# Performance work log

Hardware: AMD Instinct MI355X
Metric: run time of the kernel (lower is better)

Reference implementation:

```python
import jax, jax.numpy as jnp
import numpy as np

DIM = 2048
HEADS = 16
DIM_HEAD = 128
DIM_INNER = HEADS * DIM_HEAD
BATCH = 2
SEQ = 2048
EPS = 1e-12  # F.normalize default eps


def l2norm(t, axis=-1):
    # matches F.normalize(t, dim=axis, p=2): t / max(||t||, eps)
    n = jnp.sqrt(jnp.sum(t * t, axis=axis, keepdims=True))
    return t / jnp.maximum(n, EPS)


def setup_inputs() -> dict:
    key = jax.random.key(0)
    ks = jax.random.split(key, 5)
    x = jax.random.normal(ks[0], (BATCH, SEQ, DIM), dtype=jnp.float32)
    # NormLinear weights (torch Linear layout: [out, in]); parametrization
    # l2-normalizes rows (dim=-1) for q/k/v and columns (dim=0) for to_out.
    Wq = jax.random.normal(ks[1], (DIM_INNER, DIM), dtype=jnp.float32) / np.sqrt(DIM)
    Wk = jax.random.normal(ks[2], (DIM_INNER, DIM), dtype=jnp.float32) / np.sqrt(DIM)
    Wv = jax.random.normal(ks[3], (DIM_INNER, DIM), dtype=jnp.float32) / np.sqrt(DIM)
    Wout = jax.random.normal(ks[4], (DIM, DIM_INNER), dtype=jnp.float32) / np.sqrt(DIM_INNER)
    # Scale(dim_inner, init=1.0, scale=dim**-1): param = ones * dim**-1,
    # forward_scale = init/scale = dim, so qk_scale() starts at 1.0
    qk_scale = jnp.ones((DIM_INNER,), dtype=jnp.float32) / DIM
    return {"x": x, "Wq": Wq, "Wk": Wk, "Wv": Wv, "Wout": Wout, "qk_scale": qk_scale}


def reference(x, Wq, Wk, Wv, Wout, qk_scale):
    b, n, _ = x.shape
    # NormLinear: x @ l2norm(W, rows).T  (scale = groups**-1 = 1)
    q = jnp.einsum('bnd,ed->bne', x, l2norm(Wq, axis=-1))
    k = jnp.einsum('bnd,ed->bne', x, l2norm(Wk, axis=-1))
    v = jnp.einsum('bnd,ed->bne', x, l2norm(Wv, axis=-1))
    # split heads: b n (h d) -> b h n d
    split = lambda t: t.reshape(b, n, HEADS, DIM_HEAD).transpose(0, 2, 1, 3)
    q, k, v = split(q), split(k), split(v)
    # per-head l2norm of q and k over head dim
    q = l2norm(q, axis=-1)
    k = l2norm(k, axis=-1)
    # learned qk scale: (h d) -> h 1 d, effective = param * forward_scale(=DIM)
    q = q * (qk_scale * DIM).reshape(HEADS, 1, DIM_HEAD)
    # causal SDPA with scale = sqrt(dim_head) (unit-norm q,k in nGPT)
    attn_scale = DIM_HEAD ** 0.5
    scores = jnp.einsum('bhid,bhjd->bhij', q, k) * attn_scale
    causal = jnp.tril(jnp.ones((n, n), dtype=bool))
    scores = jnp.where(causal, scores, jnp.finfo(scores.dtype).min)
    attn = jax.nn.softmax(scores, axis=-1)
    out = jnp.einsum('bhij,bhjd->bhid', attn, v)
    # merge heads: b h n d -> b n (h d)
    out = out.transpose(0, 2, 1, 3).reshape(b, n, DIM_INNER)
    # to_out: NormLinear with norm over dim=0 of weight [DIM, DIM_INNER]
    out = jnp.einsum('bne,de->bnd', out, l2norm(Wout, axis=0))
    return out
```

## Files before the change

kernel.cpp:

```cpp
#include <hip/hip_runtime.h>


typedef __bf16 bf16x8 __attribute__((ext_vector_type(8)));
typedef float f32x4 __attribute__((ext_vector_type(4)));

__device__ __forceinline__ unsigned short f2bf(float f) {
  unsigned int u = __float_as_uint(f);
  u = u + 0x7FFFu + ((u >> 16) & 1u);
  return (unsigned short)(u >> 16);
}

__device__ __forceinline__ void async16(const void* g, void* l) {
  __builtin_amdgcn_global_load_lds(
      (const __attribute__((address_space(1))) unsigned int*)g,
      (__attribute__((address_space(3))) unsigned int*)l, 16, 0, 0);
}

#define QFOLD (2048.0f * 11.313708498984761f * 1.4426950408889634f)

__global__ __launch_bounds__(256) void prep_all(
    const float* __restrict__ x, const float* __restrict__ Wq,
    const float* __restrict__ Wk, const float* __restrict__ Wv,
    const float* __restrict__ qks, ushort* __restrict__ xbf,
    ushort* __restrict__ wqn, ushort* __restrict__ wkn,
    ushort* __restrict__ wvn, float* __restrict__ colss,
    float* __restrict__ mh) {
  const int bid = blockIdx.x;
  const int t = threadIdx.x;
  if (bid < 6144) {
    const int z = bid >> 11, row = bid & 2047;
    const float* W = (z == 0) ? Wq : (z == 1) ? Wk : Wv;
    ushort* O = (z == 0) ? wqn : (z == 1) ? wkn : wvn;
    const float4* Wr = (const float4*)(W + (size_t)row * 2048);
    float4 v0 = Wr[t];
    float4 v1 = Wr[t + 256];
    float ss = v0.x * v0.x + v0.y * v0.y + v0.z * v0.z + v0.w * v0.w +
               v1.x * v1.x + v1.y * v1.y + v1.z * v1.z + v1.w * v1.w;
    ss += __shfl_xor(ss, 1);  ss += __shfl_xor(ss, 2);
    ss += __shfl_xor(ss, 4);  ss += __shfl_xor(ss, 8);
    ss += __shfl_xor(ss, 16); ss += __shfl_xor(ss, 32);
    __shared__ float red[4];
    if ((t & 63) == 0) red[t >> 6] = ss;
    __syncthreads();
    float tot = red[0] + red[1] + red[2] + red[3];
    float sc = 1.0f / fmaxf(sqrtf(tot), 1e-12f);
    ushort4 o0, o1;
    o0.x = f2bf(v0.x * sc); o0.y = f2bf(v0.y * sc);
    o0.z = f2bf(v0.z * sc); o0.w = f2bf(v0.w * sc);
    o1.x = f2bf(v1.x * sc); o1.y = f2bf(v1.y * sc);
    o1.z = f2bf(v1.z * sc); o1.w = f2bf(v1.w * sc);
    *(ushort4*)(O + (size_t)row * 2048 + t * 4) = o0;
    *(ushort4*)(O + (size_t)row * 2048 + 1024 + t * 4) = o1;
  } else if (bid < 14336) {
    const int idx = ((bid - 6144) * 256 + t) * 4;
    float4 v = *(const float4*)(x + idx);
    ushort4 o;
    o.x = f2bf(v.x); o.y = f2bf(v.y); o.z = f2bf(v.z); o.w = f2bf(v.w);
    *(ushort4*)(xbf + idx) = o;
  } else if (bid < 14352) {
    const int h = bid - 14336;
    if (t < 64) {
      const int l = t;
      float m = fmaxf(fabsf(qks[h * 128 + l]), fabsf(qks[h * 128 + 64 + l]));
      m = fmaxf(m, __shfl_xor(m, 1));  m = fmaxf(m, __shfl_xor(m, 2));
      m = fmaxf(m, __shfl_xor(m, 4));  m = fmaxf(m, __shfl_xor(m, 8));
      m = fmaxf(m, __shfl_xor(m, 16)); m = fmaxf(m, __shfl_xor(m, 32));
      if (l == 0) mh[h] = m * QFOLD;
    }
  } else {
    float4 z4 = (float4){0.f, 0.f, 0.f, 0.f};
    ((float4*)colss)[t] = z4;
    ((float4*)colss)[t + 256] = z4;
  }
}

__global__ __launch_bounds__(256) void wout_colss(const float* __restrict__ W,
                                                  float* __restrict__ colss) {
  const int e = blockIdx.x * 256 + threadIdx.x;
  const int d0 = blockIdx.y * 128;
  float ss = 0.f;
  #pragma unroll 8
  for (int i = 0; i < 128; ++i) {
    float v = W[(size_t)(d0 + i) * 2048 + e];
    ss += v * v;
  }
  atomicAdd(colss + e, ss);
}

__global__ __launch_bounds__(256) void wout_norm(const float* __restrict__ W,
                                                 const float* __restrict__ colss,
                                                 ushort* __restrict__ O) {
  const int idx = (blockIdx.x * 256 + threadIdx.x) * 4;
  float4 v = *(const float4*)(W + idx);
  float4 c = *(const float4*)(colss + (idx & 2047));
  ushort4 o;
  o.x = f2bf(v.x / fmaxf(sqrtf(c.x), 1e-12f));
  o.y = f2bf(v.y / fmaxf(sqrtf(c.y), 1e-12f));
  o.z = f2bf(v.z / fmaxf(sqrtf(c.z), 1e-12f));
  o.w = f2bf(v.w / fmaxf(sqrtf(c.w), 1e-12f));
  *(ushort4*)(O + idx) = o;
}

__device__ __forceinline__ void gemm_mainloop(
    const ushort* __restrict__ A, const ushort* __restrict__ Bw,
    int m0, int n0, ushort* As, ushort* Bs, f32x4 acc[4][4],
    int t, int l, int wm, int wn) {
  const int l15 = l & 15, l4 = l >> 4;
  const ushort* abase = A + (size_t)m0 * 2048;
  const ushort* bbase = Bw + (size_t)n0 * 2048;
  for (int kt = 0; kt < 32; ++kt) {
    const int k0 = kt * 64;
    __syncthreads();
    #pragma unroll
    for (int p = 0; p < 9; ++p) {
      int c = p * 256 + t;
      const ushort* src = abase;
      char* dst = (char*)As;
      int cc = c;
      if (c >= 1152) { cc = c - 1152; src = bbase; dst = (char*)Bs; }
      int r = cc / 9, dc = cc - r * 9;
      int dcc = (dc == 8) ? 0 : dc;
      async16(src + (size_t)r * 2048 + k0 + dcc * 8, dst + cc * 16);
    }
    __syncthreads();
    #pragma unroll
    for (int ks = 0; ks < 2; ++ks) {
      bf16x8 af[4], bg[4];
      #pragma unroll
      for (int f = 0; f < 4; ++f)
        af[f] = *(const bf16x8*)&As[(wm * 64 + f * 16 + l15) * 72 + ks * 32 + l4 * 8];
      #pragma unroll
      for (int f = 0; f < 4; ++f)
        bg[f] = *(const bf16x8*)&Bs[(wn * 64 + f * 16 + l15) * 72 + ks * 32 + l4 * 8];
      #pragma unroll
      for (int fm = 0; fm < 4; ++fm)
        #pragma unroll
        for (int fn = 0; fn < 4; ++fn)
          acc[fm][fn] = __builtin_amdgcn_mfma_f32_16x16x32_bf16(
              af[fm], bg[fn], acc[fm][fn], 0, 0, 0);
    }
  }
}

__global__ __launch_bounds__(256, 4) void gemm_qkv(
    const ushort* __restrict__ X, const ushort* __restrict__ Wq,
    const ushort* __restrict__ Wk, const ushort* __restrict__ Wv,
    const float* __restrict__ qks, ushort* __restrict__ qn,
    ushort* __restrict__ kn, ushort* __restrict__ vt) {
  const int z = blockIdx.z;
  const ushort* Bw = (z == 0) ? Wq : (z == 1) ? Wk : Wv;
  const int n0 = blockIdx.x * 128;
  const int m0 = blockIdx.y * 128;
  __shared__ __align__(16) ushort As[128 * 72];
  __shared__ __align__(16) ushort Bs[128 * 72];
  __shared__ float partials[2][128];
  const int t = threadIdx.x, w = t >> 6, l = t & 63;
  const int wm = w & 1, wn = w >> 1;
  const int l15 = l & 15, l4 = l >> 4;

  f32x4 acc[4][4];
  #pragma unroll
  for (int i = 0; i < 4; ++i)
    #pragma unroll
    for (int j = 0; j < 4; ++j) acc[i][j] = (f32x4){0.f, 0.f, 0.f, 0.f};

  gemm_mainloop(X, Bw, m0, n0, As, Bs, acc, t, l, wm, wn);

  const int h = n0 >> 7;
  if (z == 2) {
    #pragma unroll
    for (int fm = 0; fm < 4; ++fm) {
      int mrow = m0 + wm * 64 + fm * 16 + l4 * 4;
      int bb = mrow >> 11;
      int nn = mrow & 2047;
      #pragma unroll
      for (int fn = 0; fn < 4; ++fn) {
        int d = wn * 64 + fn * 16 + l15;
        ushort4 p;
        p.x = f2bf(acc[fm][fn][0]); p.y = f2bf(acc[fm][fn][1]);
        p.z = f2bf(acc[fm][fn][2]); p.w = f2bf(acc[fm][fn][3]);
        *(ushort4*)(vt + (size_t)((bb * 16 + h) * 128 + d) * 2048 + nn) = p;
      }
    }
  } else {
    float rs[4][4];
    #pragma unroll
    for (int fm = 0; fm < 4; ++fm)
      #pragma unroll
      for (int r = 0; r < 4; ++r) {
        float s = 0.f;
        #pragma unroll
        for (int fn = 0; fn < 4; ++fn) {
          float v = acc[fm][fn][r];
          s += v * v;
        }
        s += __shfl_xor(s, 1); s += __shfl_xor(s, 2);
        s += __shfl_xor(s, 4); s += __shfl_xor(s, 8);
        rs[fm][r] = s;
      }
    if (l15 == 0) {
      #pragma unroll
      for (int fm = 0; fm < 4; ++fm)
        #pragma unroll
        for (int r = 0; r < 4; ++r)
          partials[wn][wm * 64 + fm * 16 + l4 * 4 + r] = rs[fm][r];
    }
    __syncthreads();
    float cs[4];
    #pragma unroll
    for (int fn = 0; fn < 4; ++fn)
      cs[fn] = (z == 0) ? qks[n0 + wn * 64 + fn * 16 + l15] * QFOLD : 1.0f;
    ushort* O = (z == 0) ? qn : kn;
    #pragma unroll
    for (int fm = 0; fm < 4; ++fm)
      #pragma unroll
      for (int r = 0; r < 4; ++r) {
        int i = wm * 64 + fm * 16 + l4 * 4 + r;
        float tot = partials[0][i] + partials[1][i];
        float sc = 1.0f / fmaxf(sqrtf(tot), 1e-12f);
        #pragma unroll
        for (int fn = 0; fn < 4; ++fn)
          O[(size_t)(m0 + i) * 2048 + n0 + wn * 64 + fn * 16 + l15] =
              f2bf(acc[fm][fn][r] * sc * cs[fn]);
      }
  }
}


#define LDSBUF 49152
#define ABYTES 32768

__device__ __forceinline__ void mainloop_256x128(
    const ushort* __restrict__ A, const ushort* __restrict__ Bw,
    int m0, int n0, char* lds, f32x4 acc[4][4], int t) {
  const int l = t & 63, w = t >> 6;
  const int wm = w & 3, wn = w >> 2;
  const int l15 = l & 15, l4 = l >> 4;

  const int lc = (t & 7) ^ ((t >> 3) & 7);
  const ushort* srcA = A + (size_t)m0 * 2048 + (t >> 3) * 2048 + lc * 8;
  const ushort* srcB = Bw + (size_t)n0 * 2048 + (t >> 3) * 2048 + lc * 8;
  char* dstA = lds + t * 16;
  char* dstB = lds + ABYTES + t * 16;

  const int rdA = (wm * 64 + l15) * 128;
  const int rdB = ABYTES + (wn * 64 + l15) * 128;
  const int cb0 = ((l4 ^ (l15 & 7)) * 16);
  const int cb1 = (((4 + l4) ^ (l15 & 7)) * 16);

  auto stageA = [&](int s, int k0, int o) {
    async16(srcA + (size_t)o * 131072 + k0, dstA + s * LDSBUF + o * 8192);
  };
  auto stageB = [&](int s, int k0, int o) {
    async16(srcB + (size_t)o * 131072 + k0, dstB + s * LDSBUF + o * 8192);
  };

  #pragma unroll
  for (int i = 0; i < 4; ++i)
    #pragma unroll
    for (int j = 0; j < 4; ++j) acc[i][j] = (f32x4){0.f, 0.f, 0.f, 0.f};

  stageA(0, 0, 0); stageA(0, 0, 1); stageA(0, 0, 2); stageA(0, 0, 3);
  stageB(0, 0, 0); stageB(0, 0, 1);
  stageA(1, 64, 0); stageA(1, 64, 1); stageA(1, 64, 2); stageA(1, 64, 3);
  stageB(1, 64, 0); stageB(1, 64, 1);
  asm volatile("s_waitcnt vmcnt(6)" ::: "memory");
  __builtin_amdgcn_s_barrier();

  auto tile = [&](int s, int s2, int k2, bool pf) {
    const char* Ab = lds + s * LDSBUF;
    bf16x8 af[4][2], bg[4][2];
    #pragma unroll
    for (int fm = 0; fm < 4; ++fm) {
      af[fm][0] = *(const bf16x8*)(Ab + rdA + fm * 2048 + cb0);
      af[fm][1] = *(const bf16x8*)(Ab + rdA + fm * 2048 + cb1);
    }
    #pragma unroll
    for (int fn = 0; fn < 2; ++fn) {
      bg[fn][0] = *(const bf16x8*)(Ab + rdB + fn * 2048 + cb0);
      bg[fn][1] = *(const bf16x8*)(Ab + rdB + fn * 2048 + cb1);
    }
    if (pf) { stageA(s2, k2, 0); stageA(s2, k2, 1); stageA(s2, k2, 2); }
    __builtin_amdgcn_s_setprio(1);
    #pragma unroll
    for (int ks = 0; ks < 2; ++ks)
      #pragma unroll
      for (int fm = 0; fm < 4; ++fm)
        #pragma unroll
        for (int fn = 0; fn < 2; ++fn)
          acc[fm][fn] = __builtin_amdgcn_mfma_f32_16x16x32_bf16(
              af[fm][ks], bg[fn][ks], acc[fm][fn], 0, 0, 0);
    __builtin_amdgcn_s_setprio(0);
    #pragma unroll
    for (int fn = 2; fn < 4; ++fn) {
      bg[fn][0] = *(const bf16x8*)(Ab + rdB + fn * 2048 + cb0);
      bg[fn][1] = *(const bf16x8*)(Ab + rdB + fn * 2048 + cb1);
    }
    if (pf) { stageA(s2, k2, 3); stageB(s2, k2, 0); stageB(s2, k2, 1); }
    __builtin_amdgcn_s_setprio(1);
    #pragma unroll
    for (int ks = 0; ks < 2; ++ks)
      #pragma unroll
      for (int fm = 0; fm < 4; ++fm)
        #pragma unroll
        for (int fn = 2; fn < 4; ++fn)
          acc[fm][fn] = __builtin_amdgcn_mfma_f32_16x16x32_bf16(
              af[fm][ks], bg[fn][ks], acc[fm][fn], 0, 0, 0);
    __builtin_amdgcn_s_setprio(0);
  };

  #pragma unroll 1
  for (int kt = 0; kt < 30; kt += 3) {
    tile(0, 2, (kt + 2) * 64, true);
    asm volatile("s_waitcnt vmcnt(6)" ::: "memory");
    __builtin_amdgcn_s_barrier();
    tile(1, 0, (kt + 3) * 64, true);
    asm volatile("s_waitcnt vmcnt(6)" ::: "memory");
    __builtin_amdgcn_s_barrier();
    tile(2, 1, (kt + 4) * 64, true);
    asm volatile("s_waitcnt vmcnt(6)" ::: "memory");
    __builtin_amdgcn_s_barrier();
  }
  tile(0, 0, 0, false);
  asm volatile("s_waitcnt vmcnt(0)" ::: "memory");
  __builtin_amdgcn_s_barrier();
  tile(1, 0, 0, false);
}

__global__ __launch_bounds__(256, 3) void attn_kernel(
    const ushort* __restrict__ qn, const ushort* __restrict__ kn,
    const ushort* __restrict__ vt, const float* __restrict__ mhead,
    ushort* __restrict__ ao) {
  const int hb = blockIdx.x;
  const int b = hb >> 4, h = hb & 15;
  const int qt = 31 - blockIdx.y;
  const int i0 = qt * 64;
  const int t = threadIdx.x, w = t >> 6, l = t & 63;
  const int l15 = l & 15, l4 = l >> 4;

  __shared__ __align__(16) ushort Ks[64 * 136];
  __shared__ __align__(16) ushort Vts[128 * 72];
  __shared__ __align__(16) ushort Ps[64 * 72];

  bf16x8 qf[4];
  #pragma unroll
  for (int ks = 0; ks < 4; ++ks)
    qf[ks] = *(const bf16x8*)(qn +
        (size_t)(b * 2048 + i0 + w * 16 + l15) * 2048 +
        h * 128 + ks * 32 + l4 * 8);

  f32x4 Oa[8];
  #pragma unroll
  for (int fd = 0; fd < 8; ++fd) Oa[fd] = (f32x4){0.f, 0.f, 0.f, 0.f};
  f32x4 Ol = (f32x4){0.f, 0.f, 0.f, 0.f};

  const float mh = mhead[h];
  const __bf16 one = (__bf16)1.0f;
  const bf16x8 ones = {one, one, one, one, one, one, one, one};

  const ushort* kbase = kn + (size_t)(b * 2048) * 2048 + h * 128;
  const ushort* vbase = vt + (size_t)((b * 16 + h) * 128) * 2048;

  for (int jt = 0; jt <= qt; ++jt) {
    const int j0 = jt * 64;
    __syncthreads();
    #pragma unroll
    for (int pass = 0; pass < 5; ++pass) {
      int c = pass * 256 + t;
      if (c < 1088) {
        int r = c / 17, dc = c - r * 17;
        int dcc = (dc == 16) ? 0 : dc;
        async16(kbase + (size_t)(j0 + r) * 2048 + dcc * 8, (char*)Ks + c * 16);
      }
    }
    #pragma unroll
    for (int pass = 0; pass < 5; ++pass) {
      int c = pass * 256 + t;
      if (c < 1152) {
        int r = c / 9, jc = c - r * 9;
        int jcc = (jc == 8) ? 0 : jc;
        async16(vbase + (size_t)r * 2048 + j0 + jcc * 8, (char*)Vts + c * 16);
      }
    }
    __syncthreads();

    f32x4 Sa[4];
    #pragma unroll
    for (int fj = 0; fj < 4; ++fj) {
      f32x4 s0 = (f32x4){0.f, 0.f, 0.f, 0.f};
      #pragma unroll
      for (int ks = 0; ks < 4; ++ks) {
        bf16x8 kf = *(const bf16x8*)&Ks[(fj * 16 + l15) * 136 + ks * 32 + l4 * 8];
        s0 = __builtin_amdgcn_mfma_f32_16x16x32_bf16(qf[ks], kf, s0, 0, 0, 0);
      }
      Sa[fj] = s0;
    }

    if (jt == qt) {
      #pragma unroll
      for (int fj = 0; fj < 4; ++fj)
        #pragma unroll
        for (int r = 0; r < 4; ++r) {
          int jg = fj * 16 + l15;
          int ig = w * 16 + l4 * 4 + r;
          if (jg > ig) Sa[fj][r] = -1e30f;
        }
    }

    #pragma unroll
    for (int fj = 0; fj < 4; ++fj)
      #pragma unroll
      for (int r = 0; r < 4; ++r)
        Ps[(w * 16 + l4 * 4 + r) * 72 + fj * 16 + l15] =
            f2bf(__builtin_exp2f(Sa[fj][r] - mh));

    #pragma unroll
    for (int ks = 0; ks < 2; ++ks) {
      bf16x8 p0 = *(const bf16x8*)&Ps[(w * 16 + l15) * 72 + ks * 32 + l4 * 8];
      Ol = __builtin_amdgcn_mfma_f32_16x16x32_bf16(p0, ones, Ol, 0, 0, 0);
      #pragma unroll
      for (int fd = 0; fd < 8; ++fd) {
        bf16x8 vf = *(const bf16x8*)&Vts[(fd * 16 + l15) * 72 + ks * 32 + l4 * 8];
        Oa[fd] = __builtin_amdgcn_mfma_f32_16x16x32_bf16(p0, vf, Oa[fd], 0, 0, 0);
      }
    }
  }

  #pragma unroll
  for (int r = 0; r < 4; ++r) {
    float inv = 1.0f / Ol[r];
    int ig = i0 + w * 16 + l4 * 4 + r;
    #pragma unroll
    for (int fd = 0; fd < 8; ++fd)
      ao[(size_t)(b * 2048 + ig) * 2048 + h * 128 + fd * 16 + l15] =
          f2bf(Oa[fd][r] * inv);
  }
}

__global__ __launch_bounds__(512, 2) void gemm_out(
    const ushort* __restrict__ A, const ushort* __restrict__ Bw,
    float* __restrict__ C) {
  __shared__ __align__(16) char lds[3 * LDSBUF];
  const int n0 = blockIdx.x * 128;
  const int m0 = blockIdx.y * 256;
  const int t = threadIdx.x;
  const int l = t & 63, w = t >> 6;
  const int wm = w & 3, wn = w >> 2;
  const int l15 = l & 15, l4 = l >> 4;

  f32x4 acc[4][4];
  mainloop_256x128(A, Bw, m0, n0, lds, acc, t);

  #pragma unroll
  for (int fm = 0; fm < 4; ++fm)
    #pragma unroll
    for (int fn = 0; fn < 4; ++fn)
      #pragma unroll
      for (int r = 0; r < 4; ++r)
        C[(size_t)(m0 + wm * 64 + fm * 16 + l4 * 4 + r) * 2048 +
          n0 + wn * 64 + fn * 16 + l15] = acc[fm][fn][r];
}

extern "C" void kernel_launch(void* const* d_in, const int* in_sizes, int n_in,
                              void* d_out, int out_size, void* d_ws, size_t ws_size,
                              hipStream_t stream) {
  (void)in_sizes; (void)n_in; (void)out_size; (void)ws_size;
  const float* x    = (const float*)d_in[0];
  const float* Wq   = (const float*)d_in[1];
  const float* Wk   = (const float*)d_in[2];
  const float* Wv   = (const float*)d_in[3];
  const float* Wout = (const float*)d_in[4];
  const float* qks  = (const float*)d_in[5];
  char* ws = (char*)d_ws;

  ushort* wqn  = (ushort*)(ws + 0);
  ushort* wkn  = (ushort*)(ws + 8388608);
  ushort* wvn  = (ushort*)(ws + 16777216);
  ushort* wotn = (ushort*)(ws + 25165824);
  ushort* xbf  = (ushort*)(ws + 33554432);
  ushort* qn   = (ushort*)(ws + 50331648);
  ushort* kn   = (ushort*)(ws + 67108864);
  ushort* vt   = (ushort*)(ws + 83886080);
  ushort* ao   = (ushort*)(ws + 100663296);
  float* colss = (float*)(ws + 117440512);
  float* mh    = (float*)(ws + 117448704);
  float* out   = (float*)d_out;

  prep_all<<<14353, 256, 0, stream>>>(x, Wq, Wk, Wv, qks, xbf, wqn, wkn, wvn,
                                      colss, mh);
  wout_colss<<<dim3(8, 16), 256, 0, stream>>>(Wout, colss);
  wout_norm<<<4096, 256, 0, stream>>>(Wout, colss, wotn);
  gemm_qkv<<<dim3(16, 32, 3), 256, 0, stream>>>(xbf, wqn, wkn, wvn, qks, qn, kn, vt);
  attn_kernel<<<dim3(32, 32), 256, 0, stream>>>(qn, kn, vt, mh, ao);
  gemm_out<<<dim3(16, 16), 512, 0, stream>>>(ao, wotn, out);
}
```

Before: 372.4 us.

## Fuse Q/K/V projection GEMMs into one kernel sharing the X tile

Replaces the three-slice QKV GEMM grid with one kernel per output tile that loads the X tile once and multiplies it against the Wq, Wk and Wv tiles, keeping three accumulator sets in registers. This cuts redundant X loads and LDS traffic and switches LDS to an XOR-swizzled, unpadded layout loaded with simpler address math. In exchange the kernel holds 192 accumulator floats per thread and 64KB of LDS, so occupancy drops to 2 blocks per CU and the grid is a third the size.

```diff
diff --git a/kernel.cpp b/kernel.cpp
--- a/kernel.cpp
+++ b/kernel.cpp
@@ -101,88 +101,95 @@
   *(ushort4*)(O + idx) = o;
 }
 
-__device__ __forceinline__ void gemm_mainloop(
-    const ushort* __restrict__ A, const ushort* __restrict__ Bw,
-    int m0, int n0, ushort* As, ushort* Bs, f32x4 acc[4][4],
-    int t, int l, int wm, int wn) {
-  const int l15 = l & 15, l4 = l >> 4;
-  const ushort* abase = A + (size_t)m0 * 2048;
-  const ushort* bbase = Bw + (size_t)n0 * 2048;
-  for (int kt = 0; kt < 32; ++kt) {
-    const int k0 = kt * 64;
-    __syncthreads();
-    #pragma unroll
-    for (int p = 0; p < 9; ++p) {
-      int c = p * 256 + t;
-      const ushort* src = abase;
-      char* dst = (char*)As;
-      int cc = c;
-      if (c >= 1152) { cc = c - 1152; src = bbase; dst = (char*)Bs; }
-      int r = cc / 9, dc = cc - r * 9;
-      int dcc = (dc == 8) ? 0 : dc;
-      async16(src + (size_t)r * 2048 + k0 + dcc * 8, dst + cc * 16);
-    }
-    __syncthreads();
-    #pragma unroll
-    for (int ks = 0; ks < 2; ++ks) {
-      bf16x8 af[4], bg[4];
-      #pragma unroll
-      for (int f = 0; f < 4; ++f)
-        af[f] = *(const bf16x8*)&As[(wm * 64 + f * 16 + l15) * 72 + ks * 32 + l4 * 8];
-      #pragma unroll
-      for (int f = 0; f < 4; ++f)
-        bg[f] = *(const bf16x8*)&Bs[(wn * 64 + f * 16 + l15) * 72 + ks * 32 + l4 * 8];
-      #pragma unroll
-      for (int fm = 0; fm < 4; ++fm)
-        #pragma unroll
-        for (int fn = 0; fn < 4; ++fn)
-          acc[fm][fn] = __builtin_amdgcn_mfma_f32_16x16x32_bf16(
-              af[fm], bg[fn], acc[fm][fn], 0, 0, 0);
-    }
-  }
-}
-
-__global__ __launch_bounds__(256, 4) void gemm_qkv(
+__global__ __launch_bounds__(256, 2) void gemm_qkv_fused(
     const ushort* __restrict__ X, const ushort* __restrict__ Wq,
     const ushort* __restrict__ Wk, const ushort* __restrict__ Wv,
     const float* __restrict__ qks, ushort* __restrict__ qn,
     ushort* __restrict__ kn, ushort* __restrict__ vt) {
-  const int z = blockIdx.z;
-  const ushort* Bw = (z == 0) ? Wq : (z == 1) ? Wk : Wv;
   const int n0 = blockIdx.x * 128;
   const int m0 = blockIdx.y * 128;
-  __shared__ __align__(16) ushort As[128 * 72];
-  __shared__ __align__(16) ushort Bs[128 * 72];
+  __shared__ __align__(16) char lds[4 * 16384];
   __shared__ float partials[2][128];
   const int t = threadIdx.x, w = t >> 6, l = t & 63;
   const int wm = w & 1, wn = w >> 1;
   const int l15 = l & 15, l4 = l >> 4;
 
-  f32x4 acc[4][4];
-  #pragma unroll
-  for (int i = 0; i < 4; ++i)
-    #pragma unroll
-    for (int j = 0; j < 4; ++j) acc[i][j] = (f32x4){0.f, 0.f, 0.f, 0.f};
-
-  gemm_mainloop(X, Bw, m0, n0, As, Bs, acc, t, l, wm, wn);
+  f32x4 acc[3][4][4];
+  #pragma unroll
+  for (int z = 0; z < 3; ++z)
+    #pragma unroll
+    for (int i = 0; i < 4; ++i)
+      #pragma unroll
+      for (int j = 0; j < 4; ++j) acc[z][i][j] = (f32x4){0.f, 0.f, 0.f, 0.f};
+
+  const int lc = (t & 7) ^ ((t >> 3) & 7);
+  const size_t soff = (size_t)(t >> 3) * 2048 + lc * 8;
+  const ushort* sA = X + (size_t)m0 * 2048 + soff;
+  const ushort* sQ = Wq + (size_t)n0 * 2048 + soff;
+  const ushort* sK = Wk + (size_t)n0 * 2048 + soff;
+  const ushort* sV = Wv + (size_t)n0 * 2048 + soff;
+  char* dst = lds + t * 16;
+
+  const int rdA = (wm * 64 + l15) * 128;
+  const int rdB = (wn * 64 + l15) * 128;
+  const int cb0 = (l4 ^ (l15 & 7)) * 16;
+  const int cb1 = ((4 + l4) ^ (l15 & 7)) * 16;
+
+  for (int kt = 0; kt < 32; ++kt) {
+    const int k0 = kt * 64;
+    __syncthreads();
+    #pragma unroll
+    for (int o = 0; o < 4; ++o) {
+      async16(sA + o * 65536 + k0, dst + o * 4096);
+      async16(sQ + o * 65536 + k0, dst + 16384 + o * 4096);
+      async16(sK + o * 65536 + k0, dst + 32768 + o * 4096);
+      async16(sV + o * 65536 + k0, dst + 49152 + o * 4096);
+    }
+    __syncthreads();
+    #pragma unroll
+    for (int ks = 0; ks < 2; ++ks) {
+      const int cb = ks ? cb1 : cb0;
+      bf16x8 af[4];
+      #pragma unroll
+      for (int f = 0; f < 4; ++f)
+        af[f] = *(const bf16x8*)(lds + rdA + f * 2048 + cb);
+      #pragma unroll
+      for (int z = 0; z < 3; ++z) {
+        const char* Bb = lds + 16384 * (1 + z);
+        bf16x8 bg[4];
+        #pragma unroll
+        for (int f = 0; f < 4; ++f)
+          bg[f] = *(const bf16x8*)(Bb + rdB + f * 2048 + cb);
+        #pragma unroll
+        for (int fm = 0; fm < 4; ++fm)
+          #pragma unroll
+          for (int fn = 0; fn < 4; ++fn)
+            acc[z][fm][fn] = __builtin_amdgcn_mfma_f32_16x16x32_bf16(
+                af[fm], bg[fn], acc[z][fm][fn], 0, 0, 0);
+      }
+    }
+  }
 
   const int h = n0 >> 7;
-  if (z == 2) {
-    #pragma unroll
-    for (int fm = 0; fm < 4; ++fm) {
-      int mrow = m0 + wm * 64 + fm * 16 + l4 * 4;
-      int bb = mrow >> 11;
-      int nn = mrow & 2047;
-      #pragma unroll
-      for (int fn = 0; fn < 4; ++fn) {
-        int d = wn * 64 + fn * 16 + l15;
-        ushort4 p;
-        p.x = f2bf(acc[fm][fn][0]); p.y = f2bf(acc[fm][fn][1]);
-        p.z = f2bf(acc[fm][fn][2]); p.w = f2bf(acc[fm][fn][3]);
-        *(ushort4*)(vt + (size_t)((bb * 16 + h) * 128 + d) * 2048 + nn) = p;
-      }
-    }
-  } else {
+
+  #pragma unroll
+  for (int fm = 0; fm < 4; ++fm) {
+    int mrow = m0 + wm * 64 + fm * 16 + l4 * 4;
+    int bb = mrow >> 11;
+    int nn = mrow & 2047;
+    #pragma unroll
+    for (int fn = 0; fn < 4; ++fn) {
+      int d = wn * 64 + fn * 16 + l15;
+      ushort4 p;
+      p.x = f2bf(acc[2][fm][fn][0]); p.y = f2bf(acc[2][fm][fn][1]);
+      p.z = f2bf(acc[2][fm][fn][2]); p.w = f2bf(acc[2][fm][fn][3]);
+      *(ushort4*)(vt + (size_t)((bb * 16 + h) * 128 + d) * 2048 + nn) = p;
+    }
+  }
+
+  #pragma unroll
+  for (int z = 0; z < 2; ++z) {
+    __syncthreads();
     float rs[4][4];
     #pragma unroll
     for (int fm = 0; fm < 4; ++fm)
@@ -191,7 +198,7 @@
         float s = 0.f;
         #pragma unroll
         for (int fn = 0; fn < 4; ++fn) {
-          float v = acc[fm][fn][r];
+          float v = acc[z][fm][fn][r];
           s += v * v;
         }
         s += __shfl_xor(s, 1); s += __shfl_xor(s, 2);
@@ -221,7 +228,7 @@
         #pragma unroll
         for (int fn = 0; fn < 4; ++fn)
           O[(size_t)(m0 + i) * 2048 + n0 + wn * 64 + fn * 16 + l15] =
-              f2bf(acc[fm][fn][r] * sc * cs[fn]);
+              f2bf(acc[z][fm][fn][r] * sc * cs[fn]);
       }
   }
 }
@@ -490,7 +497,8 @@
                                       colss, mh);
   wout_colss<<<dim3(8, 16), 256, 0, stream>>>(Wout, colss);
   wout_norm<<<4096, 256, 0, stream>>>(Wout, colss, wotn);
-  gemm_qkv<<<dim3(16, 32, 3), 256, 0, stream>>>(xbf, wqn, wkn, wvn, qks, qn, kn, vt);
+  gemm_qkv_fused<<<dim3(16, 32), 256, 0, stream>>>(xbf, wqn, wkn, wvn, qks,
+                                                   qn, kn, vt);
   attn_kernel<<<dim3(32, 32), 256, 0, stream>>>(qn, kn, vt, mh, ao);
   gemm_out<<<dim3(16, 16), 512, 0, stream>>>(ao, wotn, out);
 }
```

Measured after the change: 338.0 us, median of 2. 9.2% less time.
